# Performance work log

Hardware: AMD Instinct MI355X
Metric: run time of the kernel (lower is better)

The kernel has to match this reference:

```python
import jax, jax.numpy as jnp
import numpy as np

N_NODES = 100000
N_EDGES = 1600000
D_IN = 64
D_HID = 64
D_OUT = 16


def setup_inputs() -> dict:
    key = jax.random.key(0)
    k1, k2, k3, k4 = jax.random.split(key, 4)
    x = jax.random.normal(k1, (N_NODES, D_IN), dtype=jnp.float32)
    edge_index = jax.random.randint(k2, (2, N_EDGES), 0, N_NODES, dtype=jnp.int64)
    # Glorot-ish scaled weights
    W1 = jax.random.normal(k3, (D_IN, D_HID), dtype=jnp.float32) / np.sqrt(D_IN)
    b1 = jnp.zeros((D_HID,), dtype=jnp.float32)
    W2 = jax.random.normal(k4, (D_HID, D_OUT), dtype=jnp.float32) / np.sqrt(D_HID)
    b2 = jnp.zeros((D_OUT,), dtype=jnp.float32)
    return {"x": x, "edge_index": edge_index, "W1": W1, "b1": b1, "W2": W2, "b2": b2}


def _gcn_conv(x, src, dst, W, b, n_nodes):
    """PyG GCNConv: D^{-1/2} (A + I) D^{-1/2} X W + b (self-loops added)."""
    h = x @ W  # [N, F_out]
    # degree including self-loop (counted on destination, PyG default)
    deg = jnp.zeros((n_nodes,), dtype=h.dtype).at[dst].add(1.0) + 1.0
    dinv = jax.lax.rsqrt(deg)  # deg >= 1, no inf
    # edge messages: norm_e = dinv[src] * dinv[dst]
    msg = h[src] * (dinv[src] * dinv[dst])[:, None]  # [E, F_out]
    out = jax.ops.segment_sum(msg, dst, num_segments=n_nodes)
    # self-loop contribution: norm = dinv[i]^2
    out = out + h * (dinv * dinv)[:, None]
    return out + b


def reference(x, edge_index, W1, b1, W2, b2):
    src, dst = edge_index[0], edge_index[1]
    n = x.shape[0]
    h = _gcn_conv(x, src, dst, W1, b1, n)
    h = jax.nn.relu(h)
    # F.dropout(training=False) at inference -> identity
    h = _gcn_conv(h, src, dst, W2, b2, n)
    return jax.nn.log_softmax(h, axis=1)
```

## Files before the change

kernel.cpp:

```cpp
#include <hip/hip_runtime.h>
#include <hip/hip_fp16.h>
#include <math.h>

#define N_NODES 100000
#define N_EDGES 1600000
#define STRIDE 48


__global__ void k_count_fill(const int* __restrict__ src, const int* __restrict__ dst,
                             int* __restrict__ cnt, int* __restrict__ ell, int e) {
    int i = (blockIdx.x * blockDim.x + threadIdx.x) * 2;
    if (i + 2 <= e) {
        int2 d2 = *(const int2*)(dst + i);
        int2 s2 = *(const int2*)(src + i);
        int r0 = atomicAdd(&cnt[d2.x], 1);
        int r1 = atomicAdd(&cnt[d2.y], 1);
        ell[d2.x * STRIDE + r0] = s2.x;
        ell[d2.y * STRIDE + r1] = s2.y;
    } else {
        for (; i < e; ++i) {
            int d = dst[i];
            int r = atomicAdd(&cnt[d], 1);
            ell[d * STRIDE + r] = src[i];
        }
    }
}


__global__ void k_fold(const float* __restrict__ x, const int* __restrict__ cnt,
                       float* __restrict__ xs) {
    int t = blockIdx.x * blockDim.x + threadIdx.x;
    float4 v = ((const float4*)x)[t];
    float di = rsqrtf((float)cnt[t >> 4] + 1.0f);
    float4 o;
    o.x = v.x * di; o.y = v.y * di; o.z = v.z * di; o.w = v.w * di;
    ((float4*)xs)[t] = o;
}


__global__ void k_agg1(
        const float* __restrict__ xs, const int* __restrict__ cnt,
        const int* __restrict__ ell,
        const float* __restrict__ W1, const float* __restrict__ W2,
        const float* __restrict__ b1, __half* __restrict__ h2h, int n) {
    __shared__ float W1s[64 * 64];
    __shared__ float W2s[64 * 17];
    __shared__ float xsw[4][64];
    __shared__ float vsw[4][64];
    int tid = threadIdx.x;
    {
        const float4* W14 = (const float4*)W1;
        float4* W1s4 = (float4*)W1s;
#pragma unroll
        for (int i = 0; i < 4; ++i) W1s4[tid + 256 * i] = W14[tid + 256 * i];
        for (int i = tid; i < 64 * 16; i += 256) W2s[(i >> 4) * 17 + (i & 15)] = W2[i];
    }
    __syncthreads();

    int w = tid >> 6, lane = tid & 63;
    int f = lane;
    int G = lane >> 4;
    int c4 = lane & 15;
    float b1f = b1[f];

    int base = blockIdx.x * 16 + w * 4;
#pragma unroll 1
    for (int nn = 0; nn < 4; ++nn) {
        int d = base + nn;
        int deg = cnt[d];
        float dd = rsqrtf((float)deg + 1.0f);
        const int* row = ell + d * STRIDE;
        float a0 = xs[(size_t)d * 64 + f];
        float a1 = 0.f, a2 = 0.f, a3 = 0.f;
        int j = 0, je = deg;
        int s0 = 0, s1 = 0, s2 = 0, s3 = 0;
        if (j + 4 <= je) { s0 = row[0]; s1 = row[1]; s2 = row[2]; s3 = row[3]; }
        while (j + 4 <= je) {
            int t0 = s0, t1 = s1, t2 = s2, t3 = s3;
            if (j + 8 <= je) { t0 = row[j + 4]; t1 = row[j + 5]; t2 = row[j + 6]; t3 = row[j + 7]; }
            a0 += xs[(size_t)s0 * 64 + f];
            a1 += xs[(size_t)s1 * 64 + f];
            a2 += xs[(size_t)s2 * 64 + f];
            a3 += xs[(size_t)s3 * 64 + f];
            s0 = t0; s1 = t1; s2 = t2; s3 = t3;
            j += 4;
        }
        for (; j < je; ++j) {
            int s = row[j];
            a0 += xs[(size_t)s * 64 + f];
        }
        xsw[w][f] = ((a0 + a1) + (a2 + a3)) * dd;
        float p0 = b1f, p1 = 0.f, p2 = 0.f, p3 = 0.f;
        const float4* xw4 = (const float4*)xsw[w];
#pragma unroll
        for (int k4 = 0; k4 < 16; ++k4) {
            float4 xv = xw4[k4];
            p0 = fmaf(xv.x, W1s[(k4 * 4 + 0) * 64 + f], p0);
            p1 = fmaf(xv.y, W1s[(k4 * 4 + 1) * 64 + f], p1);
            p2 = fmaf(xv.z, W1s[(k4 * 4 + 2) * 64 + f], p2);
            p3 = fmaf(xv.w, W1s[(k4 * 4 + 3) * 64 + f], p3);
        }
        vsw[w][f] = fmaxf((p0 + p1) + (p2 + p3), 0.f);
        float p = 0.f;
        const float4* vw4 = (const float4*)vsw[w];
#pragma unroll
        for (int kk4 = 0; kk4 < 4; ++kk4) {
            float4 vv = vw4[G * 4 + kk4];
            p = fmaf(vv.x, W2s[(G * 16 + kk4 * 4 + 0) * 17 + c4], p);
            p = fmaf(vv.y, W2s[(G * 16 + kk4 * 4 + 1) * 17 + c4], p);
            p = fmaf(vv.z, W2s[(G * 16 + kk4 * 4 + 2) * 17 + c4], p);
            p = fmaf(vv.w, W2s[(G * 16 + kk4 * 4 + 3) * 17 + c4], p);
        }
        p += __shfl_xor(p, 16);
        p += __shfl_xor(p, 32);
        if (G == 0) h2h[(size_t)d * 16 + c4] = __float2half(p * dd);
    }
}


__global__ void k_agg2_lsm(
        const __half* __restrict__ h2h, const int* __restrict__ cnt,
        const int* __restrict__ ell,
        const float* __restrict__ b2, float* __restrict__ y, int n) {
    int tid = threadIdx.x;
    int w = tid >> 6, lane = tid & 63, g = lane >> 3, c2 = lane & 7;
    int d = blockIdx.x * 4 + w;
    const __half2* h2 = (const __half2*)h2h;
    int deg = cnt[d];
    float dd = rsqrtf((float)deg + 1.0f);
    const int* row = ell + d * STRIDE;
    float2 sv = __half22float2(h2[(size_t)d * 8 + c2]);
    float ax0 = (g == 0) ? sv.x : 0.f;
    float ay0 = (g == 0) ? sv.y : 0.f;
    float ax1 = 0.f, ay1 = 0.f;
    int j = 0, je = deg;
    for (; j + 16 <= je; j += 16) {
        int sA = row[j + g], sB = row[j + 8 + g];
        float2 vA = __half22float2(h2[(size_t)sA * 8 + c2]);
        float2 vB = __half22float2(h2[(size_t)sB * 8 + c2]);
        ax0 += vA.x; ay0 += vA.y;
        ax1 += vB.x; ay1 += vB.y;
    }
    for (; j < je; j += 8) {
        if (j + g < je) {
            int s = row[j + g];
            float2 v = __half22float2(h2[(size_t)s * 8 + c2]);
            ax0 += v.x; ay0 += v.y;
        }
    }
    float ax = ax0 + ax1, ay = ay0 + ay1;
    ax += __shfl_xor(ax, 8);  ax += __shfl_xor(ax, 16); ax += __shfl_xor(ax, 32);
    ay += __shfl_xor(ay, 8);  ay += __shfl_xor(ay, 16); ay += __shfl_xor(ay, 32);
    float vx = ax * dd + b2[c2 * 2 + 0];
    float vy = ay * dd + b2[c2 * 2 + 1];
    float m = fmaxf(vx, vy);
    m = fmaxf(m, __shfl_xor(m, 1));
    m = fmaxf(m, __shfl_xor(m, 2));
    m = fmaxf(m, __shfl_xor(m, 4));
    float ss = expf(vx - m) + expf(vy - m);
    ss += __shfl_xor(ss, 1);
    ss += __shfl_xor(ss, 2);
    ss += __shfl_xor(ss, 4);
    float lse = logf(ss) + m;
    if (g == 0) {
        float2 o; o.x = vx - lse; o.y = vy - lse;
        ((float2*)y)[(size_t)d * 8 + c2] = o;
    }
}


extern "C" void kernel_launch(void* const* d_in, const int* in_sizes, int n_in,
                              void* d_out, int out_size, void* d_ws, size_t ws_size,
                              hipStream_t stream) {
    const float* x  = (const float*)d_in[0];
    const int*   ei = (const int*)d_in[1];
    const float* W1 = (const float*)d_in[2];
    const float* b1 = (const float*)d_in[3];
    const float* W2 = (const float*)d_in[4];
    const float* b2 = (const float*)d_in[5];
    float* y = (float*)d_out;

    const int n = N_NODES;
    const int e = N_EDGES;
    const int* src = ei;
    const int* dst = ei + e;

    float* ws = (float*)d_ws;
    int*    cnt = (int*)ws;
    int*    ell = (int*)(ws + 102400);
    float*  xs  = ws + 4902400;
    __half* h2h = (__half*)(ws + 11302400);

    hipMemsetAsync(cnt, 0, (size_t)n * sizeof(int), stream);
    k_count_fill<<<(e / 2 + 255) / 256, 256, 0, stream>>>(src, dst, cnt, ell, e);
    k_fold      <<<n * 16 / 256, 256, 0, stream>>>(x, cnt, xs);
    k_agg1      <<<n / 16, 256, 0, stream>>>(xs, cnt, ell, W1, W2, b1, h2h, n);
    k_agg2_lsm  <<<n / 4, 256, 0, stream>>>(h2h, cnt, ell, b2, y, n);
}
```

Measured before the change: 317.2 us.

## Split edge count from ELL fill and co-schedule fill with degree-folding

```diff
diff --git a/kernel.cpp b/kernel.cpp
--- a/kernel.cpp
+++ b/kernel.cpp
@@ -7,34 +7,53 @@
 #define STRIDE 48
 
 
-__global__ void k_count_fill(const int* __restrict__ src, const int* __restrict__ dst,
-                             int* __restrict__ cnt, int* __restrict__ ell, int e) {
+__global__ void k_count(const int* __restrict__ dst, int* __restrict__ cnt,
+                        unsigned short* __restrict__ rnk, int e) {
     int i = (blockIdx.x * blockDim.x + threadIdx.x) * 2;
     if (i + 2 <= e) {
         int2 d2 = *(const int2*)(dst + i);
-        int2 s2 = *(const int2*)(src + i);
         int r0 = atomicAdd(&cnt[d2.x], 1);
         int r1 = atomicAdd(&cnt[d2.y], 1);
-        ell[d2.x * STRIDE + r0] = s2.x;
-        ell[d2.y * STRIDE + r1] = s2.y;
+        *(unsigned*)(rnk + i) = (unsigned)(r0 & 0xffff) | ((unsigned)r1 << 16);
     } else {
-        for (; i < e; ++i) {
-            int d = dst[i];
-            int r = atomicAdd(&cnt[d], 1);
-            ell[d * STRIDE + r] = src[i];
-        }
-    }
-}
-
-
-__global__ void k_fold(const float* __restrict__ x, const int* __restrict__ cnt,
-                       float* __restrict__ xs) {
-    int t = blockIdx.x * blockDim.x + threadIdx.x;
-    float4 v = ((const float4*)x)[t];
-    float di = rsqrtf((float)cnt[t >> 4] + 1.0f);
-    float4 o;
-    o.x = v.x * di; o.y = v.y * di; o.z = v.z * di; o.w = v.w * di;
-    ((float4*)xs)[t] = o;
+        for (; i < e; ++i) rnk[i] = (unsigned short)atomicAdd(&cnt[dst[i]], 1);
+    }
+}
+
+
+#define FILL_BLOCKS 782
+
+__global__ void k_fill_fold(const int* __restrict__ src, const int* __restrict__ dst,
+                            const unsigned short* __restrict__ rnk,
+                            int* __restrict__ ell,
+                            const float* __restrict__ x, const int* __restrict__ cnt,
+                            float* __restrict__ xs, int e) {
+    int bid = blockIdx.x;
+    if (bid < FILL_BLOCKS) {
+        int i = (bid * blockDim.x + threadIdx.x) * 8;
+        if (i + 8 <= e) {
+            int4 sA = *(const int4*)(src + i), sB = *(const int4*)(src + i + 4);
+            int4 dA = *(const int4*)(dst + i), dB = *(const int4*)(dst + i + 4);
+            int4 rp = *(const int4*)(rnk + i);
+            ell[dA.x * STRIDE + (rp.x & 0xffff)] = sA.x;
+            ell[dA.y * STRIDE + ((unsigned)rp.x >> 16)] = sA.y;
+            ell[dA.z * STRIDE + (rp.y & 0xffff)] = sA.z;
+            ell[dA.w * STRIDE + ((unsigned)rp.y >> 16)] = sA.w;
+            ell[dB.x * STRIDE + (rp.z & 0xffff)] = sB.x;
+            ell[dB.y * STRIDE + ((unsigned)rp.z >> 16)] = sB.y;
+            ell[dB.z * STRIDE + (rp.w & 0xffff)] = sB.z;
+            ell[dB.w * STRIDE + ((unsigned)rp.w >> 16)] = sB.w;
+        } else {
+            for (; i < e; ++i) ell[dst[i] * STRIDE + rnk[i]] = src[i];
+        }
+    } else {
+        int t = (bid - FILL_BLOCKS) * blockDim.x + threadIdx.x;
+        float4 v = ((const float4*)x)[t];
+        float di = rsqrtf((float)cnt[t >> 4] + 1.0f);
+        float4 o;
+        o.x = v.x * di; o.y = v.y * di; o.z = v.z * di; o.w = v.w * di;
+        ((float4*)xs)[t] = o;
+    }
 }
 
 
@@ -186,14 +205,16 @@
     const int* dst = ei + e;
 
     float* ws = (float*)d_ws;
-    int*    cnt = (int*)ws;
-    int*    ell = (int*)(ws + 102400);
-    float*  xs  = ws + 4902400;
-    __half* h2h = (__half*)(ws + 11302400);
+    int*            cnt = (int*)ws;
+    unsigned short* rnk = (unsigned short*)(ws + 102400);
+    int*            ell = (int*)(ws + 902400);
+    float*          xs  = ws + 5702400;
+    __half*         h2h = (__half*)(ws + 12102400);
 
     hipMemsetAsync(cnt, 0, (size_t)n * sizeof(int), stream);
-    k_count_fill<<<(e / 2 + 255) / 256, 256, 0, stream>>>(src, dst, cnt, ell, e);
-    k_fold      <<<n * 16 / 256, 256, 0, stream>>>(x, cnt, xs);
-    k_agg1      <<<n / 16, 256, 0, stream>>>(xs, cnt, ell, W1, W2, b1, h2h, n);
-    k_agg2_lsm  <<<n / 4, 256, 0, stream>>>(h2h, cnt, ell, b2, y, n);
-}
+    k_count<<<(e / 2 + 255) / 256, 256, 0, stream>>>(dst, cnt, rnk, e);
+    k_fill_fold<<<FILL_BLOCKS + n * 16 / 256, 256, 0, stream>>>(
+        src, dst, rnk, ell, x, cnt, xs, e);
+    k_agg1    <<<n / 16, 256, 0, stream>>>(xs, cnt, ell, W1, W2, b1, h2h, n);
+    k_agg2_lsm<<<n / 4, 256, 0, stream>>>(h2h, cnt, ell, b2, y, n);
+}
```

Result: faster. 262.3 us, median of 2 (-17.3%).
